# Kernel optimization log

Measured on AMD Instinct MI355X. Metric: run time of the kernel, lower is better.

The kernel has to match this reference:

```python
import jax, jax.numpy as jnp
import numpy as np

N, D, H, OUT, L = 4096, 127, 128, 3, 2
SIM_THRESH = 0.9
BN_EPS = 1e-5


def setup_inputs() -> dict:
    key = jax.random.key(0)
    ks = jax.random.split(key, 10)
    s = 1.0 / np.sqrt(H)
    x_now = jax.random.normal(ks[0], (N, D), dtype=jnp.float32)
    sat_type = jax.random.randint(ks[1], (N,), 0, 6, dtype=jnp.int64)
    # SAGEConv per layer: lin_l (neighbor aggr, with bias) and lin_r (root, no bias)
    Wl = jax.random.normal(ks[2], (L, H, H), dtype=jnp.float32) * s
    bl = jnp.zeros((L, H), dtype=jnp.float32)
    Wr = jax.random.normal(ks[3], (L, H, H), dtype=jnp.float32) * s
    gamma = jnp.ones((H,), dtype=jnp.float32)
    beta = jnp.zeros((H,), dtype=jnp.float32)
    Wo = jax.random.normal(ks[4], (OUT, H), dtype=jnp.float32) * s
    bo = jnp.zeros((OUT,), dtype=jnp.float32)
    return {"x_now": x_now, "sat_type": sat_type, "Wl": Wl, "bl": bl,
            "Wr": Wr, "gamma": gamma, "beta": beta, "Wo": Wo, "bo": bo}


def _forward(x_now, sat_type, Wl, bl, Wr, gamma, beta, Wo, bo):
    n = x_now.shape[0]
    # build_graph, h_prev=None branch: ppr = x_now[:, 0]
    x = jnp.concatenate([x_now[:, :1], x_now], axis=1)  # [N, H] with H = D+1
    # pairwise cosine similarity on first 4 features (F.normalize, eps=1e-12)
    f = x[:, :4]
    fn = f / jnp.maximum(jnp.linalg.norm(f, axis=1, keepdims=True), 1e-12)
    cos_sim = fn @ fn.T  # [N, N]
    same = sat_type[:, None] == sat_type[None, :]
    mask = (same | (cos_sim > SIM_THRESH)) & ~jnp.eye(n, dtype=bool)
    A = mask.astype(x.dtype)  # symmetric adjacency (dense form of edge list)
    deg = jnp.maximum(A.sum(axis=1, keepdims=True), 1.0)  # mean-aggr denom; isolated -> 0
    h = x
    for l in range(L):  # SAGEConv: lin_l(mean_j x_j) + lin_r(x_i), then ReLU
        m = (A @ h) / deg
        h = jax.nn.relu(m @ Wl[l].T + bl[l] + h @ Wr[l].T)
    # BatchNorm over nodes (training-mode batch stats, biased variance)
    mu = h.mean(axis=0)
    var = h.var(axis=0)
    h = (h - mu) / jnp.sqrt(var + BN_EPS) * gamma + beta
    out = h @ Wo.T + bo
    return h, out


def reference(x_now, sat_type, Wl, bl, Wr, gamma, beta, Wo, bo):
    return _forward(x_now, sat_type, Wl, bl, Wr, gamma, beta, Wo, bo)
```

## Files before the change

kernel.cpp:

```cpp
#include <hip/hip_runtime.h>
#include <hip/hip_bf16.h>
#include <math.h>

#define NN 4096
#define DD 127
#define HH 128
#define OUTD 3
#define NTYPES 6
#define SIM_THRESH 0.9f
#define BN_EPS 1e-5f
#define MROW 4
#define NREP 8
#define LMAXH 256

typedef unsigned short ushortT;
typedef __attribute__((ext_vector_type(8))) short short8;
typedef __attribute__((ext_vector_type(4))) float f32x4;

static __device__ inline ushortT f2bf(float f) {
    unsigned u = __float_as_uint(f);
    unsigned r = (u + 0x7fffu + ((u >> 16) & 1u)) >> 16;
    return (ushortT)r;
}

__global__ __launch_bounds__(256) void prep(
    const float* __restrict__ x_now, const int* __restrict__ sat,
    const float* __restrict__ Wl, const float* __restrict__ Wr,
    ushortT* __restrict__ Wbf, float* __restrict__ x,
    ushortT* __restrict__ xbf, float4* __restrict__ fn,
    int* __restrict__ cnt, float* __restrict__ S0rep)
{
    int t = threadIdx.x;
    if (blockIdx.x < 8) {
        int baseidx = blockIdx.x * 8192;
        #pragma unroll
        for (int it = 0; it < 32; ++it) {
            int idx = baseidx + it * 256 + t;
            float v = (idx < 32768) ? Wl[idx] : Wr[idx - 32768];
            Wbf[idx] = f2bf(v);
        }
        return;
    }

    int sb = blockIdx.x - 8;
    int base = sb * 16;
    int rep = sb & (NREP - 1);
    __shared__ int stypes[16];
    int myti = -1;
    if (t < 16) {
        int row = base + t;
        int ti = sat[row]; ti = min(max(ti, 0), NTYPES - 1);
        stypes[t] = ti; myti = ti;
        const float* rp = x_now + (size_t)row * DD;
        float f0 = rp[0], f2 = rp[1], f3 = rp[2];
        float nrm = fmaxf(sqrtf(2.f * f0 * f0 + f2 * f2 + f3 * f3), 1e-12f);
        float inv = 1.f / nrm;
        fn[row] = make_float4(f0 * inv, f0 * inv, f2 * inv, f3 * inv);
    }
    #pragma unroll
    for (int it = 0; it < 8; ++it) {
        int lin = it * 256 + t;
        int rl = lin >> 7, col = lin & 127;
        int row = base + rl;
        const float* rp = x_now + (size_t)row * DD;
        float v = (col == 0) ? rp[0] : rp[col - 1];
        x[(size_t)row * HH + col] = v;
        xbf[(size_t)row * HH + col] = f2bf(v);
    }
    __syncthreads();
    if (t < 64) {
        #pragma unroll
        for (int tt = 0; tt < NTYPES; ++tt) {
            unsigned long long m = __ballot(myti == tt);
            if (t == 0) {
                int c = __popcll(m);
                if (c) atomicAdd(&cnt[rep * NTYPES + tt], c);
            }
        }
    }
    if (t < 128) {
        float acc[NTYPES] = {0.f, 0.f, 0.f, 0.f, 0.f, 0.f};
        for (int r = 0; r < 16; ++r) {
            float v = x[(size_t)(base + r) * HH + t];
            int tt = stypes[r];
            #pragma unroll
            for (int q = 0; q < NTYPES; ++q) acc[q] += (tt == q) ? v : 0.f;
        }
        #pragma unroll
        for (int q = 0; q < NTYPES; ++q)
            atomicAdd(&S0rep[(rep * NTYPES + q) * HH + t], acc[q]);
    }
}

__global__ __launch_bounds__(256) void build_mask(
    const float4* __restrict__ fn, const int* __restrict__ sat,
    const int* __restrict__ cnt, unsigned* __restrict__ mask,
    float* __restrict__ deg)
{
    int i0 = blockIdx.x * MROW;
    int t = threadIdx.x;
    int w = t & 127;
    int half = t >> 7;
    float4 fi[MROW];
    int ti[MROW];
    #pragma unroll
    for (int r = 0; r < MROW; ++r) {
        fi[r] = fn[i0 + r];
        int tt = sat[i0 + r];
        ti[r] = min(max(tt, 0), NTYPES - 1);
    }
    unsigned word[MROW] = {0, 0, 0, 0};
    int bbase = half * 16;
    for (int bb = 0; bb < 16; ++bb) {
        int b = bbase + bb;
        int j = b * 128 + w;
        float4 fj = fn[j];
        int tj = sat[j];
        #pragma unroll
        for (int r = 0; r < MROW; ++r) {
            float dot = fi[r].x * fj.x + fi[r].y * fj.y
                      + fi[r].z * fj.z + fi[r].w * fj.w;
            if (tj != ti[r] && dot > SIM_THRESH) word[r] |= (1u << b);
        }
    }
    __shared__ unsigned wpart[MROW][128];
    if (half == 1) {
        #pragma unroll
        for (int r = 0; r < MROW; ++r) wpart[r][w] = word[r];
    }
    __syncthreads();
    __shared__ int wt[2][MROW];
    if (half == 0) {
        int pcs[MROW];
        #pragma unroll
        for (int r = 0; r < MROW; ++r) {
            unsigned full = word[r] | wpart[r][w];
            mask[(size_t)(i0 + r) * 128 + w] = full;
            pcs[r] = __popc(full);
        }
        int lane = w & 63, wv2 = w >> 6;
        for (int s = 32; s; s >>= 1) {
            #pragma unroll
            for (int r = 0; r < MROW; ++r) pcs[r] += __shfl_down(pcs[r], s);
        }
        if (lane == 0) {
            #pragma unroll
            for (int r = 0; r < MROW; ++r) wt[wv2][r] = pcs[r];
        }
    }
    __syncthreads();
    if (t < MROW) {
        int r = t;
        int ctot = 0;
        #pragma unroll
        for (int rr = 0; rr < NREP; ++rr) ctot += cnt[rr * NTYPES + ti[r]];
        float d = (float)(ctot - 1 + wt[0][r] + wt[1][r]);
        deg[i0 + r] = fmaxf(d, 1.0f);
    }
}

__global__ __launch_bounds__(256, 8) void gather_kernel(
    const float* __restrict__ h, const ushortT* __restrict__ hbf,
    const unsigned* __restrict__ mask, const float* __restrict__ deg,
    const float* __restrict__ S, const int* __restrict__ sat,
    ushortT* __restrict__ mbf)
{
    int t = threadIdx.x;
    int wv = t >> 6;
    int lane = t & 63;
    int r  = wv >> 1;
    int hf = wv & 1;
    int i0 = blockIdx.x * 2;
    int i = i0 + r;

    __shared__ ushortT list[4][LMAXH];
    __shared__ __align__(16) float hs[2][HH];
    __shared__ __align__(16) float part[4][HH];
    __shared__ int tarr[2];

    if (t < 2) {
        int tt = sat[i0 + t];
        tarr[t] = min(max(tt, 0), NTYPES - 1);
    }

    int widx = hf * 64 + lane;
    unsigned word = mask[(size_t)i * 128 + widx];
    int pc = __popc(word);
    int x = pc;
    for (int s = 1; s < 64; s <<= 1) {
        int v = __shfl_up(x, s);
        if (lane >= s) x += v;
    }
    int ncnt = __shfl(x, 63);
    int ofs = x - pc;
    unsigned ww = word;
    while (ww) {
        int b = __ffs(ww) - 1; ww &= ww - 1;
        list[wv][ofs++] = (ushortT)(b * 128 + widx);
    }
    if (hf == 0)
        ((float2*)hs[r])[lane] = ((const float2*)(h + (size_t)i * HH))[lane];

    int q = lane >> 4;
    int c = lane & 15;
    const uint4* __restrict__ hb4 = (const uint4*)hbf;
    float acc[8] = {0.f, 0.f, 0.f, 0.f, 0.f, 0.f, 0.f, 0.f};
#define BFACC(vv)                                                         \
    {                                                                     \
        acc[0] += __uint_as_float((vv).x << 16);                          \
        acc[1] += __uint_as_float((vv).x & 0xffff0000u);                  \
        acc[2] += __uint_as_float((vv).y << 16);                          \
        acc[3] += __uint_as_float((vv).y & 0xffff0000u);                  \
        acc[4] += __uint_as_float((vv).z << 16);                          \
        acc[5] += __uint_as_float((vv).z & 0xffff0000u);                  \
        acc[6] += __uint_as_float((vv).w << 16);                          \
        acc[7] += __uint_as_float((vv).w & 0xffff0000u);                  \
    }
    int g = 0;
    for (; g + 24 <= ncnt; g += 24) {
        int j0 = list[wv][g + q];
        int j1 = list[wv][g + 4 + q];
        int j2 = list[wv][g + 8 + q];
        int j3 = list[wv][g + 12 + q];
        int j4 = list[wv][g + 16 + q];
        int j5 = list[wv][g + 20 + q];
        uint4 v0 = hb4[j0 * 16 + c];
        uint4 v1 = hb4[j1 * 16 + c];
        uint4 v2 = hb4[j2 * 16 + c];
        uint4 v3 = hb4[j3 * 16 + c];
        uint4 v4 = hb4[j4 * 16 + c];
        uint4 v5 = hb4[j5 * 16 + c];
        BFACC(v0); BFACC(v1); BFACC(v2); BFACC(v3); BFACC(v4); BFACC(v5);
    }
    for (; g + 4 <= ncnt; g += 4) {
        int j0 = list[wv][g + q];
        uint4 v0 = hb4[j0 * 16 + c];
        BFACC(v0);
    }
    if (q < ncnt - g) {
        int j0 = list[wv][g + q];
        uint4 v0 = hb4[j0 * 16 + c];
        BFACC(v0);
    }
#undef BFACC
    #pragma unroll
    for (int d = 0; d < 8; ++d) {
        acc[d] += __shfl_down(acc[d], 32);
        acc[d] += __shfl_down(acc[d], 16);
    }
    if (lane < 16) {
        float4 p0 = {acc[0], acc[1], acc[2], acc[3]};
        float4 p1 = {acc[4], acc[5], acc[6], acc[7]};
        ((float4*)part[wv])[c * 2] = p0;
        ((float4*)part[wv])[c * 2 + 1] = p1;
    }
    __syncthreads();

    if (hf == 0 && lane < 32) {
        int cc = lane;
        float4 p0 = ((const float4*)part[wv])[cc];
        float4 p1 = ((const float4*)part[wv + 1])[cc];
        int ti = tarr[r];
        float rdeg = 1.f / deg[i];
        float4 hv = ((const float4*)hs[r])[cc];
        float4 Sv = {0.f, 0.f, 0.f, 0.f};
        #pragma unroll
        for (int rr = 0; rr < NREP; ++rr) {
            float4 sv = ((const float4*)S)[(rr * NTYPES + ti) * 32 + cc];
            Sv.x += sv.x; Sv.y += sv.y; Sv.z += sv.z; Sv.w += sv.w;
        }
        float4 m;
        m.x = (Sv.x - hv.x + p0.x + p1.x) * rdeg;
        m.y = (Sv.y - hv.y + p0.y + p1.y) * rdeg;
        m.z = (Sv.z - hv.z + p0.z + p1.z) * rdeg;
        m.w = (Sv.w - hv.w + p0.w + p1.w) * rdeg;
        ushort4 mb;
        mb.x = f2bf(m.x); mb.y = f2bf(m.y);
        mb.z = f2bf(m.z); mb.w = f2bf(m.w);
        ((ushort4*)(mbf + (size_t)i * HH))[cc] = mb;
    }
}

template <int MODE>
__global__ __launch_bounds__(256) void gemm_kernel(
    const ushortT* __restrict__ mbf, const ushortT* __restrict__ hbf,
    const ushortT* __restrict__ Wlbf, const ushortT* __restrict__ Wrbf,
    const float* __restrict__ bl, const int* __restrict__ sat,
    float* __restrict__ hout, ushortT* __restrict__ houtbf,
    float* __restrict__ acc0, float* __restrict__ acc1)
{
    int t = threadIdx.x;
    int wv = t >> 6, lane = t & 63;
    int p = lane & 15, q = lane >> 4;
    int i0 = blockIdx.x * 16;

    __shared__ float sh[16][129];
    __shared__ int stypes[16];
    if (t < 16) {
        int tt = sat[i0 + t];
        stypes[t] = min(max(tt, 0), NTYPES - 1);
    }

    const ushortT* arow_m = mbf + (size_t)(i0 + p) * HH + q * 8;
    const ushortT* arow_h = hbf + (size_t)(i0 + p) * HH + q * 8;
    short8 am[4], ah[4];
    #pragma unroll
    for (int s = 0; s < 4; ++s) {
        am[s] = *(const short8*)(arow_m + s * 32);
        ah[s] = *(const short8*)(arow_h + s * 32);
    }

    #pragma unroll
    for (int nt = 0; nt < 2; ++nt) {
        int n0 = (wv * 2 + nt) * 16;
        const ushortT* brow_l = Wlbf + (size_t)(n0 + p) * HH + q * 8;
        const ushortT* brow_r = Wrbf + (size_t)(n0 + p) * HH + q * 8;
        f32x4 acc = {0.f, 0.f, 0.f, 0.f};
        #pragma unroll
        for (int s = 0; s < 4; ++s) {
            short8 b = *(const short8*)(brow_l + s * 32);
            acc = __builtin_amdgcn_mfma_f32_16x16x32_bf16(am[s], b, acc, 0, 0, 0);
        }
        #pragma unroll
        for (int s = 0; s < 4; ++s) {
            short8 b = *(const short8*)(brow_r + s * 32);
            acc = __builtin_amdgcn_mfma_f32_16x16x32_bf16(ah[s], b, acc, 0, 0, 0);
        }
        int o = n0 + p;
        float bv = bl[o];
        #pragma unroll
        for (int rg = 0; rg < 4; ++rg) {
            float v = fmaxf(acc[rg] + bv, 0.f);
            sh[q * 4 + rg][o] = v;
        }
    }
    __syncthreads();

    #pragma unroll
    for (int e = 0; e < 8; ++e) {
        int lin = e * 256 + t;
        int rr = lin >> 7, cc = lin & 127;
        float v = sh[rr][cc];
        hout[(size_t)i0 * HH + lin] = v;
        if (MODE == 1) houtbf[(size_t)i0 * HH + lin] = f2bf(v);
    }
    int rep = blockIdx.x & (NREP - 1);
    if (t < HH) {
        if (MODE == 1) {
            float accq[NTYPES] = {0.f, 0.f, 0.f, 0.f, 0.f, 0.f};
            for (int r = 0; r < 16; ++r) {
                float v = sh[r][t];
                int tt = stypes[r];
                #pragma unroll
                for (int qq = 0; qq < NTYPES; ++qq)
                    accq[qq] += (tt == qq) ? v : 0.f;
            }
            #pragma unroll
            for (int qq = 0; qq < NTYPES; ++qq)
                atomicAdd(&acc0[(rep * NTYPES + qq) * HH + t], accq[qq]);
        } else {
            float s = 0.f, s2 = 0.f;
            for (int r = 0; r < 16; ++r) {
                float v = sh[r][t];
                s += v; s2 += v * v;
            }
            atomicAdd(&acc0[rep * HH + t], s);
            atomicAdd(&acc1[rep * HH + t], s2);
        }
    }
}

__global__ __launch_bounds__(256) void finalize(
    const float* __restrict__ h, const float* __restrict__ musum8,
    const float* __restrict__ varsum8, const float* __restrict__ gamma,
    const float* __restrict__ beta, const float* __restrict__ Wo,
    const float* __restrict__ bo, float* __restrict__ out_h,
    float* __restrict__ out_o)
{
    int t = threadIdx.x;
    int wv = t >> 6;
    int lane = t & 63;
    int i = blockIdx.x * 4 + wv;

    float2 mus = {0.f, 0.f}, vas = {0.f, 0.f};
    #pragma unroll
    for (int r = 0; r < NREP; ++r) {
        float2 a = ((const float2*)(musum8 + r * HH))[lane];
        float2 b = ((const float2*)(varsum8 + r * HH))[lane];
        mus.x += a.x; mus.y += a.y;
        vas.x += b.x; vas.y += b.y;
    }
    float2 ga  = ((const float2*)gamma)[lane];
    float2 be  = ((const float2*)beta)[lane];
    float mu0 = mus.x * (1.f / NN), mu1 = mus.y * (1.f / NN);
    float v0 = vas.x * (1.f / NN) - mu0 * mu0;
    float v1 = vas.y * (1.f / NN) - mu1 * mu1;
    float sc0 = ga.x / sqrtf(v0 + BN_EPS), sc1 = ga.y / sqrtf(v1 + BN_EPS);
    float sh0 = be.x - mu0 * sc0, sh1 = be.y - mu1 * sc1;

    float2 hv = ((const float2*)(h + (size_t)i * HH))[lane];
    float2 hb;
    hb.x = hv.x * sc0 + sh0;
    hb.y = hv.y * sc1 + sh1;
    ((float2*)(out_h + (size_t)i * HH))[lane] = hb;

    float2 w0 = ((const float2*)Wo)[lane];
    float2 w1 = ((const float2*)(Wo + HH))[lane];
    float2 w2 = ((const float2*)(Wo + 2 * HH))[lane];
    float p0 = hb.x * w0.x + hb.y * w0.y;
    float p1 = hb.x * w1.x + hb.y * w1.y;
    float p2 = hb.x * w2.x + hb.y * w2.y;
    for (int s = 32; s; s >>= 1) {
        p0 += __shfl_down(p0, s);
        p1 += __shfl_down(p1, s);
        p2 += __shfl_down(p2, s);
    }
    if (lane == 0) {
        out_o[(size_t)i * OUTD + 0] = p0 + bo[0];
        out_o[(size_t)i * OUTD + 1] = p1 + bo[1];
        out_o[(size_t)i * OUTD + 2] = p2 + bo[2];
    }
}

extern "C" void kernel_launch(void* const* d_in, const int* in_sizes, int n_in,
                              void* d_out, int out_size, void* d_ws, size_t ws_size,
                              hipStream_t stream)
{
    (void)in_sizes; (void)n_in; (void)out_size; (void)ws_size;
    const float* x_now = (const float*)d_in[0];
    const int*   sat   = (const int*)d_in[1];
    const float* Wl    = (const float*)d_in[2];
    const float* bl    = (const float*)d_in[3];
    const float* Wr    = (const float*)d_in[4];
    const float* gamma = (const float*)d_in[5];
    const float* beta  = (const float*)d_in[6];
    const float* Wo    = (const float*)d_in[7];
    const float* bo    = (const float*)d_in[8];

    float* ws = (float*)d_ws;
    float* x0 = ws;
    float* h1 = x0 + (size_t)NN * HH;
    float* h2 = h1 + (size_t)NN * HH;
    ushortT* Wbf  = (ushortT*)(h2 + (size_t)NN * HH);
    ushortT* x0bf = Wbf + 65536;
    ushortT* h1bf = x0bf + (size_t)NN * HH;
    ushortT* mbf  = h1bf + (size_t)NN * HH;
    float4* fn = (float4*)(mbf + (size_t)NN * HH);
    unsigned* mask = (unsigned*)((float*)fn + 4 * NN);
    float* deg = (float*)(mask + (size_t)NN * 128);
    int*   cnt   = (int*)(deg + NN);
    float* S0rep = (float*)(cnt + 64);
    float* S1rep = S0rep + NREP * NTYPES * HH;
    float* mu8   = S1rep + NREP * NTYPES * HH;
    float* var8  = mu8 + NREP * HH;

    size_t zero_bytes = (64 + 2 * NREP * NTYPES * HH + 2 * NREP * HH)
                        * sizeof(float);
    hipMemsetAsync(cnt, 0, zero_bytes, stream);

    prep<<<264, 256, 0, stream>>>(x_now, sat, Wl, Wr, Wbf, x0, x0bf, fn, cnt,
                                  S0rep);
    build_mask<<<NN / MROW, 256, 0, stream>>>(fn, sat, cnt, mask, deg);

    gather_kernel<<<NN / 2, 256, 0, stream>>>(x0, x0bf, mask, deg, S0rep, sat,
                                              mbf);
    gemm_kernel<1><<<NN / 16, 256, 0, stream>>>(
        mbf, x0bf, Wbf, Wbf + 32768, bl, sat, h1, h1bf, S1rep, nullptr);

    gather_kernel<<<NN / 2, 256, 0, stream>>>(h1, h1bf, mask, deg, S1rep, sat,
                                              mbf);
    gemm_kernel<2><<<NN / 16, 256, 0, stream>>>(
        mbf, h1bf, Wbf + 16384, Wbf + 49152, bl + HH, sat, h2, nullptr,
        mu8, var8);

    finalize<<<NN / 4, 256, 0, stream>>>(h2, mu8, var8, gamma, beta, Wo, bo,
                                         (float*)d_out, (float*)d_out + (size_t)NN * HH);
}
```

Before: 136.3 us.

## Build neighbor index lists once in build_mask and drop fp32 activation copies

build_mask now does a prefix scan and writes a compacted per-row list of cross-type neighbor indices (stride 512) plus the count. Both gather passes read these lists directly instead of each re-expanding the bitmask with ballot/ffs loops. The fp32 copies of x0 and h1 are removed: gather reads the self row from bf16 and gemm layer 1 writes only bf16. This cuts redundant mask decoding and global traffic, but the self and S0 terms now use bf16-rounded activations, and each row's list is capped at 512 entries with 256 per wave half.

```diff
diff --git a/kernel.cpp b/kernel.cpp
--- a/kernel.cpp
+++ b/kernel.cpp
@@ -11,7 +11,7 @@
 #define BN_EPS 1e-5f
 #define MROW 4
 #define NREP 8
-#define LMAXH 256
+#define GL_STRIDE 512
 
 typedef unsigned short ushortT;
 typedef __attribute__((ext_vector_type(8))) short short8;
@@ -22,13 +22,16 @@
     unsigned r = (u + 0x7fffu + ((u >> 16) & 1u)) >> 16;
     return (ushortT)r;
 }
+static __device__ inline float bf2f(ushortT b) {
+    return __uint_as_float(((unsigned)b) << 16);
+}
 
 __global__ __launch_bounds__(256) void prep(
     const float* __restrict__ x_now, const int* __restrict__ sat,
     const float* __restrict__ Wl, const float* __restrict__ Wr,
-    ushortT* __restrict__ Wbf, float* __restrict__ x,
-    ushortT* __restrict__ xbf, float4* __restrict__ fn,
-    int* __restrict__ cnt, float* __restrict__ S0rep)
+    ushortT* __restrict__ Wbf, ushortT* __restrict__ xbf,
+    float4* __restrict__ fn, int* __restrict__ cnt,
+    float* __restrict__ S0rep)
 {
     int t = threadIdx.x;
     if (blockIdx.x < 8) {
@@ -64,7 +67,6 @@
         int row = base + rl;
         const float* rp = x_now + (size_t)row * DD;
         float v = (col == 0) ? rp[0] : rp[col - 1];
-        x[(size_t)row * HH + col] = v;
         xbf[(size_t)row * HH + col] = f2bf(v);
     }
     __syncthreads();
@@ -81,7 +83,7 @@
     if (t < 128) {
         float acc[NTYPES] = {0.f, 0.f, 0.f, 0.f, 0.f, 0.f};
         for (int r = 0; r < 16; ++r) {
-            float v = x[(size_t)(base + r) * HH + t];
+            float v = bf2f(xbf[(size_t)(base + r) * HH + t]);
             int tt = stypes[r];
             #pragma unroll
             for (int q = 0; q < NTYPES; ++q) acc[q] += (tt == q) ? v : 0.f;
@@ -94,8 +96,8 @@
 
 __global__ __launch_bounds__(256) void build_mask(
     const float4* __restrict__ fn, const int* __restrict__ sat,
-    const int* __restrict__ cnt, unsigned* __restrict__ mask,
-    float* __restrict__ deg)
+    const int* __restrict__ cnt, ushortT* __restrict__ Glist,
+    int* __restrict__ ncross, float* __restrict__ deg)
 {
     int i0 = blockIdx.x * MROW;
     int t = threadIdx.x;
@@ -130,51 +132,65 @@
     }
     __syncthreads();
     __shared__ int wt[2][MROW];
+    unsigned full[MROW];
+    int pcs[MROW], xin[MROW];
+    int lane = w & 63, wv2 = w >> 6;
     if (half == 0) {
-        int pcs[MROW];
         #pragma unroll
         for (int r = 0; r < MROW; ++r) {
-            unsigned full = word[r] | wpart[r][w];
-            mask[(size_t)(i0 + r) * 128 + w] = full;
-            pcs[r] = __popc(full);
-        }
-        int lane = w & 63, wv2 = w >> 6;
-        for (int s = 32; s; s >>= 1) {
+            full[r] = word[r] | wpart[r][w];
+            pcs[r] = __popc(full[r]);
+            xin[r] = pcs[r];
+        }
+        for (int s = 1; s < 64; s <<= 1) {
             #pragma unroll
-            for (int r = 0; r < MROW; ++r) pcs[r] += __shfl_down(pcs[r], s);
-        }
-        if (lane == 0) {
+            for (int r = 0; r < MROW; ++r) {
+                int v = __shfl_up(xin[r], s);
+                if (lane >= s) xin[r] += v;
+            }
+        }
+        if (lane == 63) {
             #pragma unroll
-            for (int r = 0; r < MROW; ++r) wt[wv2][r] = pcs[r];
+            for (int r = 0; r < MROW; ++r) wt[wv2][r] = xin[r];
         }
     }
     __syncthreads();
+    if (half == 0) {
+        #pragma unroll
+        for (int r = 0; r < MROW; ++r) {
+            int excl = xin[r] - pcs[r] + (wv2 ? wt[0][r] : 0);
+            int ofs = (i0 + r) * GL_STRIDE + excl;
+            unsigned ww = full[r];
+            while (ww) {
+                int b = __ffs(ww) - 1; ww &= ww - 1;
+                Glist[ofs++] = (ushortT)(b * 128 + w);
+            }
+        }
+    }
     if (t < MROW) {
         int r = t;
+        int total = wt[0][r] + wt[1][r];
+        ncross[i0 + r] = total;
         int ctot = 0;
         #pragma unroll
         for (int rr = 0; rr < NREP; ++rr) ctot += cnt[rr * NTYPES + ti[r]];
-        float d = (float)(ctot - 1 + wt[0][r] + wt[1][r]);
-        deg[i0 + r] = fmaxf(d, 1.0f);
+        deg[i0 + r] = fmaxf((float)(ctot - 1 + total), 1.0f);
     }
 }
 
 __global__ __launch_bounds__(256, 8) void gather_kernel(
-    const float* __restrict__ h, const ushortT* __restrict__ hbf,
-    const unsigned* __restrict__ mask, const float* __restrict__ deg,
+    const ushortT* __restrict__ hbf, const ushortT* __restrict__ Glist,
+    const int* __restrict__ ncross, const float* __restrict__ deg,
     const float* __restrict__ S, const int* __restrict__ sat,
     ushortT* __restrict__ mbf)
 {
     int t = threadIdx.x;
-    int wv = t >> 6;
-    int lane = t & 63;
-    int r  = wv >> 1;
-    int hf = wv & 1;
+    int wv = t >> 6, lane = t & 63;
+    int r = wv >> 1, hf = wv & 1;
     int i0 = blockIdx.x * 2;
     int i = i0 + r;
 
-    __shared__ ushortT list[4][LMAXH];
-    __shared__ __align__(16) float hs[2][HH];
+    __shared__ ushortT idx[4][256];
     __shared__ __align__(16) float part[4][HH];
     __shared__ int tarr[2];
 
@@ -183,23 +199,16 @@
         tarr[t] = min(max(tt, 0), NTYPES - 1);
     }
 
-    int widx = hf * 64 + lane;
-    unsigned word = mask[(size_t)i * 128 + widx];
-    int pc = __popc(word);
-    int x = pc;
-    for (int s = 1; s < 64; s <<= 1) {
-        int v = __shfl_up(x, s);
-        if (lane >= s) x += v;
-    }
-    int ncnt = __shfl(x, 63);
-    int ofs = x - pc;
-    unsigned ww = word;
-    while (ww) {
-        int b = __ffs(ww) - 1; ww &= ww - 1;
-        list[wv][ofs++] = (ushortT)(b * 128 + widx);
-    }
-    if (hf == 0)
-        ((float2*)hs[r])[lane] = ((const float2*)(h + (size_t)i * HH))[lane];
+    int n = ncross[i];
+    int hcnt = (n + 1) >> 1;
+    int start = hf ? hcnt : 0;
+    int mycount = hf ? (n - hcnt) : hcnt;
+    const ushortT* gl = Glist + (size_t)i * GL_STRIDE + start;
+    #pragma unroll
+    for (int b = 0; b < 4; ++b) {
+        int ii = b * 64 + lane;
+        if (ii < mycount) idx[wv][ii] = gl[ii];
+    }
 
     int q = lane >> 4;
     int c = lane & 15;
@@ -217,13 +226,13 @@
         acc[7] += __uint_as_float((vv).w & 0xffff0000u);                  \
     }
     int g = 0;
-    for (; g + 24 <= ncnt; g += 24) {
-        int j0 = list[wv][g + q];
-        int j1 = list[wv][g + 4 + q];
-        int j2 = list[wv][g + 8 + q];
-        int j3 = list[wv][g + 12 + q];
-        int j4 = list[wv][g + 16 + q];
-        int j5 = list[wv][g + 20 + q];
+    for (; g + 24 <= mycount; g += 24) {
+        int j0 = idx[wv][g + q];
+        int j1 = idx[wv][g + 4 + q];
+        int j2 = idx[wv][g + 8 + q];
+        int j3 = idx[wv][g + 12 + q];
+        int j4 = idx[wv][g + 16 + q];
+        int j5 = idx[wv][g + 20 + q];
         uint4 v0 = hb4[j0 * 16 + c];
         uint4 v1 = hb4[j1 * 16 + c];
         uint4 v2 = hb4[j2 * 16 + c];
@@ -232,13 +241,13 @@
         uint4 v5 = hb4[j5 * 16 + c];
         BFACC(v0); BFACC(v1); BFACC(v2); BFACC(v3); BFACC(v4); BFACC(v5);
     }
-    for (; g + 4 <= ncnt; g += 4) {
-        int j0 = list[wv][g + q];
+    for (; g + 4 <= mycount; g += 4) {
+        int j0 = idx[wv][g + q];
         uint4 v0 = hb4[j0 * 16 + c];
         BFACC(v0);
     }
-    if (q < ncnt - g) {
-        int j0 = list[wv][g + q];
+    if (q < mycount - g) {
+        int j0 = idx[wv][g + q];
         uint4 v0 = hb4[j0 * 16 + c];
         BFACC(v0);
     }
@@ -262,7 +271,12 @@
         float4 p1 = ((const float4*)part[wv + 1])[cc];
         int ti = tarr[r];
         float rdeg = 1.f / deg[i];
-        float4 hv = ((const float4*)hs[r])[cc];
+        uint2 hu = ((const uint2*)(hbf + (size_t)i * HH))[cc];
+        float4 hv;
+        hv.x = __uint_as_float(hu.x << 16);
+        hv.y = __uint_as_float(hu.x & 0xffff0000u);
+        hv.z = __uint_as_float(hu.y << 16);
+        hv.w = __uint_as_float(hu.y & 0xffff0000u);
         float4 Sv = {0.f, 0.f, 0.f, 0.f};
         #pragma unroll
         for (int rr = 0; rr < NREP; ++rr) {
@@ -341,8 +355,8 @@
         int lin = e * 256 + t;
         int rr = lin >> 7, cc = lin & 127;
         float v = sh[rr][cc];
-        hout[(size_t)i0 * HH + lin] = v;
         if (MODE == 1) houtbf[(size_t)i0 * HH + lin] = f2bf(v);
+        else          hout[(size_t)i0 * HH + lin] = v;
     }
     int rep = blockIdx.x & (NREP - 1);
     if (t < HH) {
@@ -438,37 +452,36 @@
     const float* bo    = (const float*)d_in[8];
 
     float* ws = (float*)d_ws;
-    float* x0 = ws;
-    float* h1 = x0 + (size_t)NN * HH;
-    float* h2 = h1 + (size_t)NN * HH;
-    ushortT* Wbf  = (ushortT*)(h2 + (size_t)NN * HH);
-    ushortT* x0bf = Wbf + 65536;
-    ushortT* h1bf = x0bf + (size_t)NN * HH;
-    ushortT* mbf  = h1bf + (size_t)NN * HH;
-    float4* fn = (float4*)(mbf + (size_t)NN * HH);
-    unsigned* mask = (unsigned*)((float*)fn + 4 * NN);
-    float* deg = (float*)(mask + (size_t)NN * 128);
-    int*   cnt   = (int*)(deg + NN);
-    float* S0rep = (float*)(cnt + 64);
-    float* S1rep = S0rep + NREP * NTYPES * HH;
-    float* mu8   = S1rep + NREP * NTYPES * HH;
-    float* var8  = mu8 + NREP * HH;
+    float*  h2     = ws;
+    float4* fn     = (float4*)(h2 + (size_t)NN * HH);
+    float*  deg    = (float*)(fn + NN);
+    int*    ncross = (int*)(deg + NN);
+    int*    cnt    = ncross + NN;
+    float*  S0rep  = (float*)(cnt + 64);
+    float*  S1rep  = S0rep + NREP * NTYPES * HH;
+    float*  mu8    = S1rep + NREP * NTYPES * HH;
+    float*  var8   = mu8 + NREP * HH;
+    ushortT* Wbf   = (ushortT*)(var8 + NREP * HH);
+    ushortT* x0bf  = Wbf + 65536;
+    ushortT* h1bf  = x0bf + (size_t)NN * HH;
+    ushortT* mbf   = h1bf + (size_t)NN * HH;
+    ushortT* Glist = mbf + (size_t)NN * HH;
 
     size_t zero_bytes = (64 + 2 * NREP * NTYPES * HH + 2 * NREP * HH)
                         * sizeof(float);
     hipMemsetAsync(cnt, 0, zero_bytes, stream);
 
-    prep<<<264, 256, 0, stream>>>(x_now, sat, Wl, Wr, Wbf, x0, x0bf, fn, cnt,
+    prep<<<264, 256, 0, stream>>>(x_now, sat, Wl, Wr, Wbf, x0bf, fn, cnt,
                                   S0rep);
-    build_mask<<<NN / MROW, 256, 0, stream>>>(fn, sat, cnt, mask, deg);
-
-    gather_kernel<<<NN / 2, 256, 0, stream>>>(x0, x0bf, mask, deg, S0rep, sat,
-                                              mbf);
+    build_mask<<<NN / MROW, 256, 0, stream>>>(fn, sat, cnt, Glist, ncross, deg);
+
+    gather_kernel<<<NN / 2, 256, 0, stream>>>(x0bf, Glist, ncross, deg, S0rep,
+                                              sat, mbf);
     gemm_kernel<1><<<NN / 16, 256, 0, stream>>>(
-        mbf, x0bf, Wbf, Wbf + 32768, bl, sat, h1, h1bf, S1rep, nullptr);
-
-    gather_kernel<<<NN / 2, 256, 0, stream>>>(h1, h1bf, mask, deg, S1rep, sat,
-                                              mbf);
+        mbf, x0bf, Wbf, Wbf + 32768, bl, sat, nullptr, h1bf, S1rep, nullptr);
+
+    gather_kernel<<<NN / 2, 256, 0, stream>>>(h1bf, Glist, ncross, deg, S1rep,
+                                              sat, mbf);
     gemm_kernel<2><<<NN / 16, 256, 0, stream>>>(
         mbf, h1bf, Wbf + 16384, Wbf + 49152, bl + HH, sat, h2, nullptr,
         mu8, var8);
```

After: 138.1 us. About the same (+1.4%).
